# Optimization experiments

Measured on AMD Instinct MI355X. Metric: run time of the kernel, lower is better.

Reference implementation:

```python
import jax, jax.numpy as jnp
import numpy as np

N_NODES = 100000
N_EDGES = 3200000
IN_DIM, HID_DIM, OUT_DIM = 256, 64, 32


def setup_inputs() -> dict:
    key = jax.random.key(0)
    ks = jax.random.split(key, 12)
    s = 0.05
    x = jax.random.normal(ks[0], (N_NODES, IN_DIM), dtype=jnp.float32)
    edge_index = jax.random.randint(ks[1], (2, N_EDGES), 0, N_NODES, dtype=jnp.int64)
    return {
        "x": x,
        "edge_index": edge_index,
        # GCNConv 1: in->hid
        "W1": jax.random.normal(ks[2], (IN_DIM, HID_DIM), dtype=jnp.float32) * s,
        "b1": jnp.zeros((HID_DIM,), dtype=jnp.float32),
        # GCNConv 2: hid->out
        "W2": jax.random.normal(ks[3], (HID_DIM, OUT_DIM), dtype=jnp.float32) * s,
        "b2": jnp.zeros((OUT_DIM,), dtype=jnp.float32),
        # weight_predictor MLP: Linear(out,hid) -> ReLU -> Linear(hid,1) -> Sigmoid
        "Wp1": jax.random.normal(ks[4], (OUT_DIM, HID_DIM), dtype=jnp.float32) * s,
        "bp1": jnp.zeros((HID_DIM,), dtype=jnp.float32),
        "Wp2": jax.random.normal(ks[5], (HID_DIM, 1), dtype=jnp.float32) * s,
        "bp2": jnp.zeros((1,), dtype=jnp.float32),
    }


def gcn_conv(h, src, dst, deg_norm, W, b, n_nodes):
    """PyG GCNConv: x' = D^-1/2 (A+I) D^-1/2 (x W) + b, edges incl. self-loops."""
    h = h @ W                                   # [N, F_out]
    coef = deg_norm[src] * deg_norm[dst]        # [E+N]
    agg = jax.ops.segment_sum(h[src] * coef[:, None], dst, num_segments=n_nodes)
    return agg + b


def reference(x, edge_index, W1, b1, W2, b2, Wp1, bp1, Wp2, bp2):
    n = x.shape[0]
    loop = jnp.arange(n, dtype=edge_index.dtype)
    src = jnp.concatenate([edge_index[0], loop])  # self-loops appended
    dst = jnp.concatenate([edge_index[1], loop])
    # degree (with self-loops) on target nodes, deg^-1/2 with inf->0
    deg = jax.ops.segment_sum(jnp.ones_like(dst, dtype=x.dtype), dst, num_segments=n)
    deg_norm = jnp.where(deg > 0, jax.lax.rsqrt(deg), 0.0)

    h = gcn_conv(x, src, dst, deg_norm, W1, b1, n)
    h = jax.nn.relu(h)                            # dropout inactive (eval)
    h = gcn_conv(h, src, dst, deg_norm, W2, b2, n)  # no relu after last conv

    # weight predictor MLP head
    p = jax.nn.relu(h @ Wp1 + bp1)
    node_weights = jax.nn.sigmoid(p @ Wp2 + bp2)  # [N, 1]
    return h, node_weights
```

## Files before the change

kernel.cpp:

```cpp
#include <hip/hip_runtime.h>
#include <hip/hip_bf16.h>
#include <cstdint>
#include <cstddef>

#define N_NODES 100000
#define N_EDGES 3200000
#define IN_DIM  256
#define HID_DIM 64
#define OUT_DIM 32

#define NBINS      391
#define BIN_SHIFT  8
#define BIN_STRIDE 9216
#define BIN_EPB    8192

typedef unsigned int uint;
typedef unsigned char uchar;

#define SMEM_BYTES 50176

__global__ __launch_bounds__(512)
void k_bin_gemm(const int* __restrict__ ei, int* __restrict__ bin_cursor,
                uint* __restrict__ binned, int* __restrict__ bin_base,
                int* __restrict__ rowptr,
                const float* __restrict__ X, const float* __restrict__ W,
                float* __restrict__ Y) {
    __shared__ __align__(16) char smem[SMEM_BYTES];
    const int bid = blockIdx.x;
    const int tid = threadIdx.x;

    if (bid < NBINS) {
        int*   lcount = (int*)(smem);
        int*   lstart = (int*)(smem + 1564);
        int*   lplace = (int*)(smem + 3128);
        int*   gbase  = (int*)(smem + 4692);
        int*   sc     = (int*)(smem + 6256);
        uint*  stage  = (uint*)(smem + 8304);
        uchar* binid  = (uchar*)(smem + 41072);
        int*   done   = bin_cursor + NBINS;

        const int e0   = bid * BIN_EPB;
        const int nval = min(BIN_EPB, N_EDGES - e0);

        for (int i = tid; i < NBINS; i += 512) lcount[i] = 0;
        __syncthreads();

        #pragma unroll
        for (int k = 0; k < BIN_EPB / 512; ++k) {
            int e = e0 + k * 512 + tid;
            if (e < N_EDGES) atomicAdd(&lcount[ei[N_EDGES + e] >> BIN_SHIFT], 1);
        }
        __syncthreads();

        int v = (tid < NBINS) ? lcount[tid] : 0;
        sc[tid] = v; __syncthreads();
        for (int off = 1; off < 512; off <<= 1) {
            int x = sc[tid];
            if (tid >= off) x += sc[tid - off];
            __syncthreads(); sc[tid] = x; __syncthreads();
        }
        if (tid < NBINS) {
            int excl = sc[tid] - v;
            lstart[tid] = excl;
            lplace[tid] = excl;
            gbase[tid]  = atomicAdd(&bin_cursor[tid], v);
        }
        __syncthreads();

        #pragma unroll
        for (int k = 0; k < BIN_EPB / 512; ++k) {
            int e = e0 + k * 512 + tid;
            if (e < N_EDGES) {
                int s = ei[e];
                int d = ei[N_EDGES + e];
                int b = d >> BIN_SHIFT;
                int p = atomicAdd(&lplace[b], 1);
                stage[p] = (uint)s | ((uint)(d & 255) << 17) | ((uint)(b >> 8) << 25);
                binid[p] = (uchar)(b & 255);
            }
        }
        __syncthreads();

        for (int i = tid; i < nval; i += 512) {
            uint ed = stage[i];
            int  b  = (int)binid[i] | (int)((ed >> 25) & 1u) << 8;
            int  gix = gbase[b] + (i - lstart[b]);
            if (gix < BIN_STRIDE)
                binned[(size_t)b * BIN_STRIDE + gix] = ed;
        }
        __syncthreads();

        if (tid == 0) {
            __threadfence();
            lcount[0] = (atomicAdd(done, 1) == NBINS - 1) ? 1 : 0;
        }
        __syncthreads();
        if (lcount[0]) {
            int t = tid;
            int vv = 0;
            if (t < NBINS) vv = min(atomicAdd(&bin_cursor[t], 0), BIN_STRIDE);
            sc[t] = vv; __syncthreads();
            for (int off = 1; off < 512; off <<= 1) {
                int x = sc[t];
                if (t >= off) x += sc[t - off];
                __syncthreads(); sc[t] = x; __syncthreads();
            }
            if (t < NBINS)      bin_base[t] = sc[t] - vv;
            if (t == NBINS - 1) rowptr[N_NODES] = sc[t];
        }
    } else {
        constexpr int KD = IN_DIM, NC = HID_DIM, KC = 32;
        const int half = tid >> 8;
        const int lt   = tid & 255;
        float* Xs = (float*)(smem) + half * 128 * 33;
        float* Ws = (float*)(smem + 33792) + half * KC * NC;
        const int tr   = lt / 8;
        const int tc   = lt % 8;
        const int row0 = ((bid - NBINS) * 2 + half) * 128;
        const int M    = N_NODES;

        float acc[4][8];
        #pragma unroll
        for (int i = 0; i < 4; ++i)
            #pragma unroll
            for (int j = 0; j < 8; ++j) acc[i][j] = 0.f;

        for (int kc = 0; kc < KD; kc += KC) {
            #pragma unroll
            for (int i = lt; i < 128 * (KC / 4); i += 256) {
                int r  = i / (KC / 4);
                int k4 = (i % (KC / 4)) * 4;
                float4 vv = make_float4(0.f, 0.f, 0.f, 0.f);
                int gr = row0 + r;
                if (gr < M)
                    vv = *reinterpret_cast<const float4*>(&X[(size_t)gr * KD + kc + k4]);
                Xs[r * 33 + k4 + 0] = vv.x; Xs[r * 33 + k4 + 1] = vv.y;
                Xs[r * 33 + k4 + 2] = vv.z; Xs[r * 33 + k4 + 3] = vv.w;
            }
            #pragma unroll
            for (int i = lt; i < KC * (NC / 4); i += 256) {
                int kk = i / (NC / 4);
                int c4 = (i % (NC / 4)) * 4;
                *reinterpret_cast<float4*>(&Ws[kk * NC + c4]) =
                    *reinterpret_cast<const float4*>(&W[(size_t)(kc + kk) * NC + c4]);
            }
            __syncthreads();

            #pragma unroll
            for (int kk = 0; kk < KC; ++kk) {
                float xv[4];
                #pragma unroll
                for (int i = 0; i < 4; ++i) xv[i] = Xs[(tr * 4 + i) * 33 + kk];
                float4 w0 = *reinterpret_cast<const float4*>(&Ws[kk * NC + tc * 8]);
                float4 w1 = *reinterpret_cast<const float4*>(&Ws[kk * NC + tc * 8 + 4]);
                float wv[8] = {w0.x, w0.y, w0.z, w0.w, w1.x, w1.y, w1.z, w1.w};
                #pragma unroll
                for (int i = 0; i < 4; ++i)
                    #pragma unroll
                    for (int j = 0; j < 8; ++j)
                        acc[i][j] = fmaf(xv[i], wv[j], acc[i][j]);
            }
            __syncthreads();
        }

        #pragma unroll
        for (int i = 0; i < 4; ++i) {
            int gr = row0 + tr * 4 + i;
            if (gr < M) {
                float4 o0 = make_float4(acc[i][0], acc[i][1], acc[i][2], acc[i][3]);
                float4 o1 = make_float4(acc[i][4], acc[i][5], acc[i][6], acc[i][7]);
                *reinterpret_cast<float4*>(&Y[(size_t)gr * NC + tc * 8])     = o0;
                *reinterpret_cast<float4*>(&Y[(size_t)gr * NC + tc * 8 + 4]) = o1;
            }
        }
    }
}

__global__ __launch_bounds__(256)
void k_csr(const uint* __restrict__ binned, const int* __restrict__ bin_cursor,
           const int* __restrict__ bin_base, int* __restrict__ rowptr,
           float* __restrict__ dn, int* __restrict__ csr) {
    __shared__ int lcnt[256];
    __shared__ int lpl[256];
    __shared__ int sc[256];
    __shared__ int csr_s[BIN_STRIDE];

    const int tid   = threadIdx.x;
    const int b     = blockIdx.x;
    const int n0    = b << BIN_SHIFT;
    const int cnt   = min(bin_cursor[b], BIN_STRIDE);
    const int ebase = bin_base[b];
    const uint* bb  = binned + (size_t)b * BIN_STRIDE;

    lcnt[tid] = 0;
    __syncthreads();
    for (int i = tid; i < cnt; i += 256)
        atomicAdd(&lcnt[(bb[i] >> 17) & 255u], 1);
    __syncthreads();

    int v = lcnt[tid];
    sc[tid] = v; __syncthreads();
    for (int off = 1; off < 256; off <<= 1) {
        int x = sc[tid];
        if (tid >= off) x += sc[tid - off];
        __syncthreads(); sc[tid] = x; __syncthreads();
    }
    int excl = sc[tid] - v;
    lpl[tid] = excl;
    int n = n0 + tid;
    if (n < N_NODES) {
        rowptr[n] = ebase + excl;
        dn[n]     = rsqrtf((float)v + 1.0f);
    }
    __syncthreads();

    for (int i = tid; i < cnt; i += 256) {
        uint ed = bb[i];
        int  p  = atomicAdd(&lpl[(ed >> 17) & 255u], 1);
        csr_s[p] = (int)(ed & 0x1FFFFu);
    }
    __syncthreads();
    for (int i = tid; i < cnt; i += 256)
        csr[ebase + i] = csr_s[i];
}

__global__ __launch_bounds__(256)
void k_agg1(const float* __restrict__ H1, const int* __restrict__ rowptr,
            const int* __restrict__ csr, const float* __restrict__ dn,
            const float* __restrict__ b1, const float* __restrict__ W2,
            float* __restrict__ H2) {
    __shared__ float W2s[HID_DIM * OUT_DIM];
    for (int i = threadIdx.x; i < HID_DIM * OUT_DIM; i += 256) W2s[i] = W2[i];
    __syncthreads();

    int wid  = (blockIdx.x * blockDim.x + threadIdx.x) >> 6;
    int lane = threadIdx.x & 63;
    if (wid >= N_NODES / 2) return;
    const int half = lane >> 5;
    const int hb   = half << 5;
    const int l    = lane & 31;
    const int n    = 2 * wid + half;

    int rp = (l < 2) ? rowptr[n + l] : 0;
    int base = __shfl(rp, hb + 0);
    int cnt  = __shfl(rp, hb + 1) - base;
    const float dnn = dn[n];

    float2 self2 = *reinterpret_cast<const float2*>(H1 + (size_t)n * HID_DIM + 2 * l);
    float2 acc;
    acc.x = dnn * self2.x;
    acc.y = dnn * self2.y;

    const int cnt2 = max(cnt, __shfl_xor(cnt, 32));
    for (int b0 = 0; b0 < cnt2; b0 += 32) {
        int m_own = min(32, cnt - b0);
        int m_max = min(32, cnt2 - b0);
        int s = 0; float dsv = 0.f;
        if (l < m_own) { s = csr[base + b0 + l]; dsv = dn[s]; }
        for (int j0 = 0; j0 < m_max; j0 += 8) {
            float2 v[8]; float w[8];
            #pragma unroll
            for (int i = 0; i < 8; ++i) {
                int j  = j0 + i;
                int sj = __shfl(s, hb + j);
                w[i] = __shfl(dsv, hb + j);
                v[i] = *reinterpret_cast<const float2*>(H1 + (size_t)sj * HID_DIM + 2 * l);
            }
            #pragma unroll
            for (int i = 0; i < 8; ++i) {
                acc.x = fmaf(w[i], v[i].x, acc.x);
                acc.y = fmaf(w[i], v[i].y, acc.y);
            }
        }
    }
    float2 b1q = *reinterpret_cast<const float2*>(b1 + 2 * l);
    float2 o;
    o.x = fmaxf(b1q.x + dnn * acc.x, 0.f);
    o.y = fmaxf(b1q.y + dnn * acc.y, 0.f);

    const int c = lane & 31, hh = lane >> 5;
    #pragma unroll
    for (int nodesel = 0; nodesel < 2; ++nodesel) {
        const int nb = nodesel << 5;
        float acc2 = 0.f;
        #pragma unroll
        for (int fi = 0; fi < 32; ++fi) {
            int f = hh * 32 + fi;
            float vv = (f & 1) ? __shfl(o.y, nb + (f >> 1))
                               : __shfl(o.x, nb + (f >> 1));
            acc2 = fmaf(vv, W2s[f * OUT_DIM + c], acc2);
        }
        acc2 += __shfl_xor(acc2, 32);
        if (hh == 0) H2[(size_t)(2 * wid + nodesel) * OUT_DIM + c] = acc2;
    }
}

__global__ __launch_bounds__(256)
void k_agg2m(const float* __restrict__ H2, const int* __restrict__ rowptr,
             const int* __restrict__ csr, const float* __restrict__ dn,
             const float* __restrict__ b2, const float* __restrict__ Wp1,
             const float* __restrict__ bp1, const float* __restrict__ Wp2,
             const float* __restrict__ bp2, float* __restrict__ out_h,
             float* __restrict__ out_w) {
    __shared__ float Wp1s[OUT_DIM * HID_DIM];
    __shared__ float Wp2s[HID_DIM];
    __shared__ float bp1s[HID_DIM];
    for (int i = threadIdx.x; i < OUT_DIM * HID_DIM; i += 256) Wp1s[i] = Wp1[i];
    if (threadIdx.x < HID_DIM) {
        Wp2s[threadIdx.x] = Wp2[threadIdx.x];
        bp1s[threadIdx.x] = bp1[threadIdx.x];
    }
    __syncthreads();

    int wid  = (blockIdx.x * blockDim.x + threadIdx.x) >> 6;
    int lane = threadIdx.x & 63;
    if (wid >= N_NODES) return;
    const int n = wid;

    int rp = (lane < 2) ? rowptr[n + lane] : 0;
    int base = __shfl(rp, 0);
    int cnt  = __shfl(rp, 1) - base;
    const float dnn = dn[n];
    const int f = lane & 31, h = lane >> 5;

    float acc = (h == 0) ? dnn * H2[(size_t)n * OUT_DIM + f] : 0.f;
    for (int b0 = 0; b0 < cnt; b0 += 64) {
        int m = min(64, cnt - b0);
        int s = 0; float dsv = 0.f;
        if (lane < m) { s = csr[base + b0 + lane]; dsv = dn[s]; }
        for (int j0 = h; j0 < m; j0 += 16) {
            float v[8], w[8];
            #pragma unroll
            for (int i = 0; i < 8; ++i) {
                int j  = j0 + 2 * i;
                int sj = __shfl(s, j);
                w[i] = __shfl(dsv, j);
                v[i] = H2[(size_t)sj * OUT_DIM + f];
            }
            #pragma unroll
            for (int i = 0; i < 8; ++i) acc = fmaf(w[i], v[i], acc);
        }
    }
    acc += __shfl_xor(acc, 32);
    float hv = b2[f] + dnn * acc;
    if (h == 0) out_h[(size_t)n * OUT_DIM + f] = hv;

    float p = bp1s[lane];
    #pragma unroll
    for (int ff = 0; ff < OUT_DIM; ++ff) {
        float hf = __shfl(hv, ff);
        p = fmaf(hf, Wp1s[ff * HID_DIM + lane], p);
    }
    p = fmaxf(p, 0.f);
    float z = p * Wp2s[lane];
    #pragma unroll
    for (int off = 32; off; off >>= 1) z += __shfl_xor(z, off);
    if (lane == 0) out_w[n] = 1.f / (1.f + __expf(-(z + bp2[0])));
}

extern "C" void kernel_launch(void* const* d_in, const int* in_sizes, int n_in,
                              void* d_out, int out_size, void* d_ws, size_t ws_size,
                              hipStream_t stream) {
    const float* x   = (const float*)d_in[0];
    const int*   ei  = (const int*)d_in[1];
    const float* W1  = (const float*)d_in[2];
    const float* b1  = (const float*)d_in[3];
    const float* W2  = (const float*)d_in[4];
    const float* b2  = (const float*)d_in[5];
    const float* Wp1 = (const float*)d_in[6];
    const float* bp1 = (const float*)d_in[7];
    const float* Wp2 = (const float*)d_in[8];
    const float* bp2 = (const float*)d_in[9];
    float* out = (float*)d_out;

    char* ws = (char*)d_ws;
    int*   bin_cursor = (int*)  (ws + 0);
    int*   bin_base   = (int*)  (ws + 2048);
    int*   rowptr     = (int*)  (ws + 4096);
    float* dn         = (float*)(ws + 404480);
    int*   csr        = (int*)  (ws + 804608);
    uint*  binned     = (uint*) (ws + 13604608);
    float* H1         = (float*)(ws + 28018432);
    float* H2         = (float*)(ws + 53618432);

    hipMemsetAsync(bin_cursor, 0, (NBINS + 1) * sizeof(int), stream);

    k_bin_gemm<<<NBINS + 391, 512, 0, stream>>>(ei, bin_cursor, binned, bin_base,
                                                rowptr, x, W1, H1);
    k_csr<<<NBINS, 256, 0, stream>>>(binned, bin_cursor, bin_base, rowptr, dn, csr);

    k_agg1<<<(N_NODES / 2 + 3) / 4, 256, 0, stream>>>(H1, rowptr, csr, dn, b1, W2, H2);
    k_agg2m<<<(N_NODES + 3) / 4, 256, 0, stream>>>(H2, rowptr, csr, dn, b2,
                                                   Wp1, bp1, Wp2, bp2,
                                                   out, out + (size_t)N_NODES * OUT_DIM);
}
```

Measured before the change: 338.4 us.

## Split fused bin/GEMM kernel and process two nodes per wave in agg2

The fused binning+GEMM kernel is split back into a separate edge-binning kernel and a templated 256-thread GEMM kernel launched one after the other. The second aggregation kernel now handles two nodes per 64-lane wave, with each half-wave reading float2 feature slices for one node. The MLP head is then evaluated for both nodes in the wave. This is meant to use all lanes during the 32-wide gather and halve the wave count. In exchange, it gives up the overlap between binning and GEMM, and divergence grows when the two nodes have unequal degrees.

```diff
diff --git a/kernel.cpp b/kernel.cpp
--- a/kernel.cpp
+++ b/kernel.cpp
@@ -17,161 +17,160 @@
 typedef unsigned int uint;
 typedef unsigned char uchar;
 
-#define SMEM_BYTES 50176
-
 __global__ __launch_bounds__(512)
-void k_bin_gemm(const int* __restrict__ ei, int* __restrict__ bin_cursor,
-                uint* __restrict__ binned, int* __restrict__ bin_base,
-                int* __restrict__ rowptr,
-                const float* __restrict__ X, const float* __restrict__ W,
-                float* __restrict__ Y) {
-    __shared__ __align__(16) char smem[SMEM_BYTES];
-    const int bid = blockIdx.x;
-    const int tid = threadIdx.x;
-
-    if (bid < NBINS) {
-        int*   lcount = (int*)(smem);
-        int*   lstart = (int*)(smem + 1564);
-        int*   lplace = (int*)(smem + 3128);
-        int*   gbase  = (int*)(smem + 4692);
-        int*   sc     = (int*)(smem + 6256);
-        uint*  stage  = (uint*)(smem + 8304);
-        uchar* binid  = (uchar*)(smem + 41072);
-        int*   done   = bin_cursor + NBINS;
-
-        const int e0   = bid * BIN_EPB;
-        const int nval = min(BIN_EPB, N_EDGES - e0);
-
-        for (int i = tid; i < NBINS; i += 512) lcount[i] = 0;
+void k_bin(const int* __restrict__ ei, int* __restrict__ bin_cursor,
+           uint* __restrict__ binned, int* __restrict__ bin_base,
+           int* __restrict__ rowptr) {
+    __shared__ int   lcount[NBINS];
+    __shared__ int   lstart[NBINS];
+    __shared__ int   lplace[NBINS];
+    __shared__ int   gbase[NBINS];
+    __shared__ int   sc[512];
+    __shared__ uint  stage[BIN_EPB];
+    __shared__ uchar binid[BIN_EPB];
+
+    const int tid  = threadIdx.x;
+    const int bid  = blockIdx.x;
+    int*      done = bin_cursor + NBINS;
+
+    const int e0   = bid * BIN_EPB;
+    const int nval = min(BIN_EPB, N_EDGES - e0);
+
+    for (int i = tid; i < NBINS; i += 512) lcount[i] = 0;
+    __syncthreads();
+
+    #pragma unroll
+    for (int k = 0; k < BIN_EPB / 512; ++k) {
+        int e = e0 + k * 512 + tid;
+        if (e < N_EDGES) atomicAdd(&lcount[ei[N_EDGES + e] >> BIN_SHIFT], 1);
+    }
+    __syncthreads();
+
+    int v = (tid < NBINS) ? lcount[tid] : 0;
+    sc[tid] = v; __syncthreads();
+    for (int off = 1; off < 512; off <<= 1) {
+        int x = sc[tid];
+        if (tid >= off) x += sc[tid - off];
+        __syncthreads(); sc[tid] = x; __syncthreads();
+    }
+    if (tid < NBINS) {
+        int excl = sc[tid] - v;
+        lstart[tid] = excl;
+        lplace[tid] = excl;
+        gbase[tid]  = atomicAdd(&bin_cursor[tid], v);
+    }
+    __syncthreads();
+
+    #pragma unroll
+    for (int k = 0; k < BIN_EPB / 512; ++k) {
+        int e = e0 + k * 512 + tid;
+        if (e < N_EDGES) {
+            int s = ei[e];
+            int d = ei[N_EDGES + e];
+            int b = d >> BIN_SHIFT;
+            int p = atomicAdd(&lplace[b], 1);
+            stage[p] = (uint)s | ((uint)(d & 255) << 17) | ((uint)(b >> 8) << 25);
+            binid[p] = (uchar)(b & 255);
+        }
+    }
+    __syncthreads();
+
+    for (int i = tid; i < nval; i += 512) {
+        uint ed = stage[i];
+        int  b  = (int)binid[i] | (int)((ed >> 25) & 1u) << 8;
+        int  gix = gbase[b] + (i - lstart[b]);
+        if (gix < BIN_STRIDE)
+            binned[(size_t)b * BIN_STRIDE + gix] = ed;
+    }
+    __syncthreads();
+
+    if (tid == 0) {
+        __threadfence();
+        lcount[0] = (atomicAdd(done, 1) == gridDim.x - 1) ? 1 : 0;
+    }
+    __syncthreads();
+    if (lcount[0]) {
+        int t = tid;
+        int vv = 0;
+        if (t < NBINS) vv = min(atomicAdd(&bin_cursor[t], 0), BIN_STRIDE);
+        sc[t] = vv; __syncthreads();
+        for (int off = 1; off < 512; off <<= 1) {
+            int x = sc[t];
+            if (t >= off) x += sc[t - off];
+            __syncthreads(); sc[t] = x; __syncthreads();
+        }
+        if (t < NBINS)      bin_base[t] = sc[t] - vv;
+        if (t == NBINS - 1) rowptr[N_NODES] = sc[t];
+    }
+}
+
+template<int KD, int NC>
+__global__ __launch_bounds__(32 * (NC / 8))
+void k_gemm(const float* __restrict__ X, const float* __restrict__ W,
+            float* __restrict__ Y, int M) {
+    constexpr int TC = NC / 8;
+    constexpr int THREADS = 32 * TC;
+    constexpr int KC = 32;
+    __shared__ float Xs[128][33];
+    __shared__ float Ws[KC][NC];
+
+    const int tid  = threadIdx.x;
+    const int tr   = tid / TC;
+    const int tc   = tid % TC;
+    const int row0 = blockIdx.x * 128;
+
+    float acc[4][8];
+    #pragma unroll
+    for (int i = 0; i < 4; ++i)
+        #pragma unroll
+        for (int j = 0; j < 8; ++j) acc[i][j] = 0.f;
+
+    for (int kc = 0; kc < KD; kc += KC) {
+        #pragma unroll
+        for (int i = tid; i < 128 * (KC / 4); i += THREADS) {
+            int r  = i / (KC / 4);
+            int k4 = (i % (KC / 4)) * 4;
+            float4 v = make_float4(0.f, 0.f, 0.f, 0.f);
+            int gr = row0 + r;
+            if (gr < M)
+                v = *reinterpret_cast<const float4*>(&X[(size_t)gr * KD + kc + k4]);
+            Xs[r][k4 + 0] = v.x; Xs[r][k4 + 1] = v.y;
+            Xs[r][k4 + 2] = v.z; Xs[r][k4 + 3] = v.w;
+        }
+        #pragma unroll
+        for (int i = tid; i < KC * (NC / 4); i += THREADS) {
+            int kk = i / (NC / 4);
+            int c4 = (i % (NC / 4)) * 4;
+            *reinterpret_cast<float4*>(&Ws[kk][c4]) =
+                *reinterpret_cast<const float4*>(&W[(size_t)(kc + kk) * NC + c4]);
+        }
         __syncthreads();
 
         #pragma unroll
-        for (int k = 0; k < BIN_EPB / 512; ++k) {
-            int e = e0 + k * 512 + tid;
-            if (e < N_EDGES) atomicAdd(&lcount[ei[N_EDGES + e] >> BIN_SHIFT], 1);
+        for (int kk = 0; kk < KC; ++kk) {
+            float xv[4];
+            #pragma unroll
+            for (int i = 0; i < 4; ++i) xv[i] = Xs[tr * 4 + i][kk];
+            float4 w0 = *reinterpret_cast<const float4*>(&Ws[kk][tc * 8]);
+            float4 w1 = *reinterpret_cast<const float4*>(&Ws[kk][tc * 8 + 4]);
+            float wv[8] = {w0.x, w0.y, w0.z, w0.w, w1.x, w1.y, w1.z, w1.w};
+            #pragma unroll
+            for (int i = 0; i < 4; ++i)
+                #pragma unroll
+                for (int j = 0; j < 8; ++j)
+                    acc[i][j] = fmaf(xv[i], wv[j], acc[i][j]);
         }
         __syncthreads();
-
-        int v = (tid < NBINS) ? lcount[tid] : 0;
-        sc[tid] = v; __syncthreads();
-        for (int off = 1; off < 512; off <<= 1) {
-            int x = sc[tid];
-            if (tid >= off) x += sc[tid - off];
-            __syncthreads(); sc[tid] = x; __syncthreads();
-        }
-        if (tid < NBINS) {
-            int excl = sc[tid] - v;
-            lstart[tid] = excl;
-            lplace[tid] = excl;
-            gbase[tid]  = atomicAdd(&bin_cursor[tid], v);
-        }
-        __syncthreads();
-
-        #pragma unroll
-        for (int k = 0; k < BIN_EPB / 512; ++k) {
-            int e = e0 + k * 512 + tid;
-            if (e < N_EDGES) {
-                int s = ei[e];
-                int d = ei[N_EDGES + e];
-                int b = d >> BIN_SHIFT;
-                int p = atomicAdd(&lplace[b], 1);
-                stage[p] = (uint)s | ((uint)(d & 255) << 17) | ((uint)(b >> 8) << 25);
-                binid[p] = (uchar)(b & 255);
-            }
-        }
-        __syncthreads();
-
-        for (int i = tid; i < nval; i += 512) {
-            uint ed = stage[i];
-            int  b  = (int)binid[i] | (int)((ed >> 25) & 1u) << 8;
-            int  gix = gbase[b] + (i - lstart[b]);
-            if (gix < BIN_STRIDE)
-                binned[(size_t)b * BIN_STRIDE + gix] = ed;
-        }
-        __syncthreads();
-
-        if (tid == 0) {
-            __threadfence();
-            lcount[0] = (atomicAdd(done, 1) == NBINS - 1) ? 1 : 0;
-        }
-        __syncthreads();
-        if (lcount[0]) {
-            int t = tid;
-            int vv = 0;
-            if (t < NBINS) vv = min(atomicAdd(&bin_cursor[t], 0), BIN_STRIDE);
-            sc[t] = vv; __syncthreads();
-            for (int off = 1; off < 512; off <<= 1) {
-                int x = sc[t];
-                if (t >= off) x += sc[t - off];
-                __syncthreads(); sc[t] = x; __syncthreads();
-            }
-            if (t < NBINS)      bin_base[t] = sc[t] - vv;
-            if (t == NBINS - 1) rowptr[N_NODES] = sc[t];
-        }
-    } else {
-        constexpr int KD = IN_DIM, NC = HID_DIM, KC = 32;
-        const int half = tid >> 8;
-        const int lt   = tid & 255;
-        float* Xs = (float*)(smem) + half * 128 * 33;
-        float* Ws = (float*)(smem + 33792) + half * KC * NC;
-        const int tr   = lt / 8;
-        const int tc   = lt % 8;
-        const int row0 = ((bid - NBINS) * 2 + half) * 128;
-        const int M    = N_NODES;
-
-        float acc[4][8];
-        #pragma unroll
-        for (int i = 0; i < 4; ++i)
-            #pragma unroll
-            for (int j = 0; j < 8; ++j) acc[i][j] = 0.f;
-
-        for (int kc = 0; kc < KD; kc += KC) {
-            #pragma unroll
-            for (int i = lt; i < 128 * (KC / 4); i += 256) {
-                int r  = i / (KC / 4);
-                int k4 = (i % (KC / 4)) * 4;
-                float4 vv = make_float4(0.f, 0.f, 0.f, 0.f);
-                int gr = row0 + r;
-                if (gr < M)
-                    vv = *reinterpret_cast<const float4*>(&X[(size_t)gr * KD + kc + k4]);
-                Xs[r * 33 + k4 + 0] = vv.x; Xs[r * 33 + k4 + 1] = vv.y;
-                Xs[r * 33 + k4 + 2] = vv.z; Xs[r * 33 + k4 + 3] = vv.w;
-            }
-            #pragma unroll
-            for (int i = lt; i < KC * (NC / 4); i += 256) {
-                int kk = i / (NC / 4);
-                int c4 = (i % (NC / 4)) * 4;
-                *reinterpret_cast<float4*>(&Ws[kk * NC + c4]) =
-                    *reinterpret_cast<const float4*>(&W[(size_t)(kc + kk) * NC + c4]);
-            }
-            __syncthreads();
-
-            #pragma unroll
-            for (int kk = 0; kk < KC; ++kk) {
-                float xv[4];
-                #pragma unroll
-                for (int i = 0; i < 4; ++i) xv[i] = Xs[(tr * 4 + i) * 33 + kk];
-                float4 w0 = *reinterpret_cast<const float4*>(&Ws[kk * NC + tc * 8]);
-                float4 w1 = *reinterpret_cast<const float4*>(&Ws[kk * NC + tc * 8 + 4]);
-                float wv[8] = {w0.x, w0.y, w0.z, w0.w, w1.x, w1.y, w1.z, w1.w};
-                #pragma unroll
-                for (int i = 0; i < 4; ++i)
-                    #pragma unroll
-                    for (int j = 0; j < 8; ++j)
-                        acc[i][j] = fmaf(xv[i], wv[j], acc[i][j]);
-            }
-            __syncthreads();
-        }
-
-        #pragma unroll
-        for (int i = 0; i < 4; ++i) {
-            int gr = row0 + tr * 4 + i;
-            if (gr < M) {
-                float4 o0 = make_float4(acc[i][0], acc[i][1], acc[i][2], acc[i][3]);
-                float4 o1 = make_float4(acc[i][4], acc[i][5], acc[i][6], acc[i][7]);
-                *reinterpret_cast<float4*>(&Y[(size_t)gr * NC + tc * 8])     = o0;
-                *reinterpret_cast<float4*>(&Y[(size_t)gr * NC + tc * 8 + 4]) = o1;
-            }
+    }
+
+    #pragma unroll
+    for (int i = 0; i < 4; ++i) {
+        int gr = row0 + tr * 4 + i;
+        if (gr < M) {
+            float4 o0 = make_float4(acc[i][0], acc[i][1], acc[i][2], acc[i][3]);
+            float4 o1 = make_float4(acc[i][4], acc[i][5], acc[i][6], acc[i][7]);
+            *reinterpret_cast<float4*>(&Y[(size_t)gr * NC + tc * 8])     = o0;
+            *reinterpret_cast<float4*>(&Y[(size_t)gr * NC + tc * 8 + 4]) = o1;
         }
     }
 }
@@ -314,48 +313,72 @@
 
     int wid  = (blockIdx.x * blockDim.x + threadIdx.x) >> 6;
     int lane = threadIdx.x & 63;
-    if (wid >= N_NODES) return;
-    const int n = wid;
-
-    int rp = (lane < 2) ? rowptr[n + lane] : 0;
-    int base = __shfl(rp, 0);
-    int cnt  = __shfl(rp, 1) - base;
+    if (wid >= N_NODES / 2) return;
+    const int nd  = lane >> 5;
+    const int nb0 = nd << 5;
+    const int l32 = lane & 31;
+    const int l   = lane & 15;
+    const int h2  = (lane >> 4) & 1;
+    const int n   = 2 * wid + nd;
+
+    int rp = (lane < 3) ? rowptr[2 * wid + lane] : 0;
+    int base = __shfl(rp, nd);
+    int cnt  = __shfl(rp, nd + 1) - base;
     const float dnn = dn[n];
-    const int f = lane & 31, h = lane >> 5;
-
-    float acc = (h == 0) ? dnn * H2[(size_t)n * OUT_DIM + f] : 0.f;
-    for (int b0 = 0; b0 < cnt; b0 += 64) {
-        int m = min(64, cnt - b0);
+
+    float2 self2 = *reinterpret_cast<const float2*>(H2 + (size_t)n * OUT_DIM + 2 * l);
+    float2 acc;
+    acc.x = (h2 == 0) ? dnn * self2.x : 0.f;
+    acc.y = (h2 == 0) ? dnn * self2.y : 0.f;
+
+    const int cnt2 = max(cnt, __shfl_xor(cnt, 32));
+    for (int b0 = 0; b0 < cnt2; b0 += 32) {
+        int m_own = min(32, cnt - b0);
+        int m_max = min(32, cnt2 - b0);
         int s = 0; float dsv = 0.f;
-        if (lane < m) { s = csr[base + b0 + lane]; dsv = dn[s]; }
-        for (int j0 = h; j0 < m; j0 += 16) {
-            float v[8], w[8];
+        if (l32 < m_own) { s = csr[base + b0 + l32]; dsv = dn[s]; }
+        for (int j0 = h2; j0 < m_max; j0 += 16) {
+            float2 v[8]; float w[8];
             #pragma unroll
             for (int i = 0; i < 8; ++i) {
                 int j  = j0 + 2 * i;
-                int sj = __shfl(s, j);
-                w[i] = __shfl(dsv, j);
-                v[i] = H2[(size_t)sj * OUT_DIM + f];
+                int sj = __shfl(s, nb0 + j);
+                w[i] = __shfl(dsv, nb0 + j);
+                v[i] = *reinterpret_cast<const float2*>(H2 + (size_t)sj * OUT_DIM + 2 * l);
             }
             #pragma unroll
-            for (int i = 0; i < 8; ++i) acc = fmaf(w[i], v[i], acc);
-        }
-    }
-    acc += __shfl_xor(acc, 32);
-    float hv = b2[f] + dnn * acc;
-    if (h == 0) out_h[(size_t)n * OUT_DIM + f] = hv;
-
-    float p = bp1s[lane];
-    #pragma unroll
-    for (int ff = 0; ff < OUT_DIM; ++ff) {
-        float hf = __shfl(hv, ff);
-        p = fmaf(hf, Wp1s[ff * HID_DIM + lane], p);
-    }
-    p = fmaxf(p, 0.f);
-    float z = p * Wp2s[lane];
-    #pragma unroll
-    for (int off = 32; off; off >>= 1) z += __shfl_xor(z, off);
-    if (lane == 0) out_w[n] = 1.f / (1.f + __expf(-(z + bp2[0])));
+            for (int i = 0; i < 8; ++i) {
+                acc.x = fmaf(w[i], v[i].x, acc.x);
+                acc.y = fmaf(w[i], v[i].y, acc.y);
+            }
+        }
+    }
+    acc.x += __shfl_xor(acc.x, 16);
+    acc.y += __shfl_xor(acc.y, 16);
+    float2 b2q = *reinterpret_cast<const float2*>(b2 + 2 * l);
+    float2 hv;
+    hv.x = b2q.x + dnn * acc.x;
+    hv.y = b2q.y + dnn * acc.y;
+    if (h2 == 0)
+        *reinterpret_cast<float2*>(out_h + (size_t)n * OUT_DIM + 2 * l) = hv;
+
+    #pragma unroll
+    for (int nodesel = 0; nodesel < 2; ++nodesel) {
+        const int nb = nodesel << 5;
+        float p = bp1s[lane];
+        #pragma unroll
+        for (int ff = 0; ff < OUT_DIM; ++ff) {
+            float hf = (ff & 1) ? __shfl(hv.y, nb + (ff >> 1))
+                                : __shfl(hv.x, nb + (ff >> 1));
+            p = fmaf(hf, Wp1s[ff * HID_DIM + lane], p);
+        }
+        p = fmaxf(p, 0.f);
+        float z = p * Wp2s[lane];
+        #pragma unroll
+        for (int off = 32; off; off >>= 1) z += __shfl_xor(z, off);
+        if (lane == 0)
+            out_w[2 * wid + nodesel] = 1.f / (1.f + __expf(-(z + bp2[0])));
+    }
 }
 
 extern "C" void kernel_launch(void* const* d_in, const int* in_sizes, int n_in,
@@ -385,12 +408,13 @@
 
     hipMemsetAsync(bin_cursor, 0, (NBINS + 1) * sizeof(int), stream);
 
-    k_bin_gemm<<<NBINS + 391, 512, 0, stream>>>(ei, bin_cursor, binned, bin_base,
-                                                rowptr, x, W1, H1);
+    k_bin<<<(N_EDGES + BIN_EPB - 1) / BIN_EPB, 512, 0, stream>>>(ei, bin_cursor, binned,
+                                                                 bin_base, rowptr);
+    k_gemm<IN_DIM, HID_DIM><<<(N_NODES + 127) / 128, 256, 0, stream>>>(x, W1, H1, N_NODES);
     k_csr<<<NBINS, 256, 0, stream>>>(binned, bin_cursor, bin_base, rowptr, dn, csr);
 
     k_agg1<<<(N_NODES / 2 + 3) / 4, 256, 0, stream>>>(H1, rowptr, csr, dn, b1, W2, H2);
-    k_agg2m<<<(N_NODES + 3) / 4, 256, 0, stream>>>(H2, rowptr, csr, dn, b2,
-                                                   Wp1, bp1, Wp2, bp2,
-                                                   out, out + (size_t)N_NODES * OUT_DIM);
-}
+    k_agg2m<<<(N_NODES / 2 + 3) / 4, 256, 0, stream>>>(H2, rowptr, csr, dn, b2,
+                                                       Wp1, bp1, Wp2, bp2,
+                                                       out, out + (size_t)N_NODES * OUT_DIM);
+}
```

Result: faster. 321.1 us (-5.1%).
